# Performance work log

Hardware: AMD Instinct MI355X
Metric: run time of the kernel (lower is better)

The kernel has to match this reference:

```python
import jax, jax.numpy as jnp
import numpy as np

N = 65536   # batch_size * timeseries
D = 512     # feature dim of h_real
K = 64      # n_clusters


def setup_inputs() -> dict:
    key = jax.random.key(0)
    k1, k2 = jax.random.split(key)
    h_real = jax.random.normal(k1, (N, D), dtype=jnp.float32)
    # F is an (approximately) orthogonal projection parameter [N, K].
    F = jax.random.normal(k2, (N, K), dtype=jnp.float32)
    return {"h_real": h_real, "F": F}


def reference(h_real, F):
    # Original: WTW = h h^T (N x N); loss = trace(WTW) - trace(F^T WTW F).
    # Algebraically identical reduced form, never materializing the N x N Gram:
    #   trace(h h^T) = sum(h * h)
    #   trace(F^T h h^T F) = ||F^T h||_F^2
    tr_wtw = jnp.sum(h_real * h_real)
    G = F.T @ h_real                      # [K, D] skinny GEMM
    tr_proj = jnp.sum(G * G)
    return tr_wtw - tr_proj
```

## Files before the change

### kernel.cpp

```cpp
#include <hip/hip_runtime.h>
#include <hip/hip_fp16.h>

#define N_TOT 65536
#define D_DIM 512
#define K_DIM 64
#define NC    32
#define HT_S  40
#define GSZ   (K_DIM * D_DIM)

typedef __bf16   bf16x8 __attribute__((ext_vector_type(8)));
typedef float    f32x4  __attribute__((ext_vector_type(4)));
typedef _Float16 half8  __attribute__((ext_vector_type(8)));

__device__ __forceinline__ unsigned int pack_bf16(float a, float b) {
    union { float f; unsigned int u; } x, y;
    x.f = a; y.f = b;
    unsigned int lo = (x.u + 0x7fffu + ((x.u >> 16) & 1u)) >> 16;
    unsigned int hi = (y.u + 0x7fffu + ((y.u >> 16) & 1u)) >> 16;
    return lo | (hi << 16);
}

extern "C" __global__ void __launch_bounds__(1024)
k1_partial(const float* __restrict__ h, const float* __restrict__ F,
           float* __restrict__ trw_out, unsigned short* __restrict__ gpart,
           float* __restrict__ out, int rowsPerBlock) {
    __shared__ unsigned short ht[2][D_DIM * HT_S];
    __shared__ unsigned short Ft[2][K_DIM * HT_S];
    __shared__ float red[16];

    const int tid = threadIdx.x;
    const int b   = blockIdx.x;
    if (b == 0 && tid == 0) out[0] = 0.0f;

    const int row0    = b * rowsPerBlock;
    const int nChunks = rowsPerBlock / NC;

    const int sd = tid & 511;
    const int sg = tid >> 9;
    const int fk = tid & 63;
    const int fg = (tid >> 6) & 3;
    const int wave = tid >> 6;
    const int lane = tid & 63;
    const int m    = lane & 15;
    const int q    = lane >> 4;

    f32x4 acc[4][2];
    #pragma unroll
    for (int kt = 0; kt < 4; ++kt)
        #pragma unroll
        for (int dt = 0; dt < 2; ++dt)
            acc[kt][dt] = (f32x4){0.f, 0.f, 0.f, 0.f};

    float trw = 0.f;

    auto stage = [&](int c, int p) {
        const int r0 = row0 + c * NC;
        const float* hb = h + (size_t)r0 * D_DIM + sd;
        #pragma unroll
        for (int gi = 0; gi < 2; ++gi) {
            const int g8 = gi * 2 + sg;
            float v[8];
            #pragma unroll
            for (int j = 0; j < 8; ++j) {
                v[j] = hb[(size_t)(g8 * 8 + j) * D_DIM];
                trw += v[j] * v[j];
            }
            uint4 pk;
            pk.x = pack_bf16(v[0], v[1]);
            pk.y = pack_bf16(v[2], v[3]);
            pk.z = pack_bf16(v[4], v[5]);
            pk.w = pack_bf16(v[6], v[7]);
            *(uint4*)&ht[p][sd * HT_S + g8 * 8] = pk;
        }
        if (tid < 256) {
            const float* fb = F + (size_t)r0 * K_DIM + fk;
            float w[8];
            #pragma unroll
            for (int j = 0; j < 8; ++j)
                w[j] = fb[(size_t)(fg * 8 + j) * K_DIM];
            uint4 pk;
            pk.x = pack_bf16(w[0], w[1]);
            pk.y = pack_bf16(w[2], w[3]);
            pk.z = pack_bf16(w[4], w[5]);
            pk.w = pack_bf16(w[6], w[7]);
            *(uint4*)&Ft[p][fk * HT_S + fg * 8] = pk;
        }
    };

    stage(0, 0);

    for (int c = 0; c < nChunks; ++c) {
        __syncthreads();
        if (c + 1 < nChunks) stage(c + 1, (c + 1) & 1);

        const int p = c & 1;
        bf16x8 bfrag[2], afrag[4];
        #pragma unroll
        for (int dt = 0; dt < 2; ++dt)
            bfrag[dt] = *(const bf16x8*)&ht[p][(wave * 32 + dt * 16 + m) * HT_S + q * 8];
        #pragma unroll
        for (int kt = 0; kt < 4; ++kt)
            afrag[kt] = *(const bf16x8*)&Ft[p][(kt * 16 + m) * HT_S + q * 8];
        #pragma unroll
        for (int kt = 0; kt < 4; ++kt)
            #pragma unroll
            for (int dt = 0; dt < 2; ++dt)
                acc[kt][dt] = __builtin_amdgcn_mfma_f32_16x16x32_bf16(
                    afrag[kt], bfrag[dt], acc[kt][dt], 0, 0, 0);
    }

    unsigned short* gp = gpart + (size_t)b * GSZ;
    #pragma unroll
    for (int kt = 0; kt < 4; ++kt)
        #pragma unroll
        for (int dt = 0; dt < 2; ++dt)
            #pragma unroll
            for (int r = 0; r < 4; ++r) {
                const int k = kt * 16 + q * 4 + r;
                const int d = wave * 32 + dt * 16 + m;
                __half hv = __float2half(acc[kt][dt][r]);
                gp[k * D_DIM + d] = *(unsigned short*)&hv;
            }

    #pragma unroll
    for (int off = 32; off > 0; off >>= 1) trw += __shfl_down(trw, off, 64);
    if (lane == 0) red[wave] = trw;
    __syncthreads();
    if (tid == 0) {
        float s = 0.f;
        #pragma unroll
        for (int w = 0; w < 16; ++w) s += red[w];
        trw_out[b] = s;
    }
}

extern "C" __global__ void __launch_bounds__(512)
k2_reduce(const float* __restrict__ trw, const unsigned short* __restrict__ gpart,
          float* __restrict__ out, int P) {
    __shared__ float sh[32 * 16 * 8];
    __shared__ float red2[8];

    const int tid = threadIdx.x;
    const int sub = tid >> 4;
    const int oct = tid & 15;
    const int tt  = blockIdx.x * 16 + oct;

    float g[8];
    #pragma unroll
    for (int j = 0; j < 8; ++j) g[j] = 0.f;

    const unsigned short* base = gpart + (size_t)tt * 8;
    for (int b = sub; b < P; b += 32) {
        half8 v = *(const half8*)(base + (size_t)b * GSZ);
        #pragma unroll
        for (int j = 0; j < 8; ++j) g[j] += (float)v[j];
    }
    #pragma unroll
    for (int j = 0; j < 8; ++j) sh[(sub * 16 + oct) * 8 + j] = g[j];
    __syncthreads();

    float val = 0.f;
    if (tid < 128) {
        const int o2 = tid >> 3, j = tid & 7;
        float s = 0.f;
        #pragma unroll
        for (int sb = 0; sb < 32; ++sb) s += sh[(sb * 16 + o2) * 8 + j];
        val = -s * s;
    } else if (blockIdx.x == 0 && tid - 128 < P) {
        val = trw[tid - 128];
    }

    #pragma unroll
    for (int off = 32; off > 0; off >>= 1) val += __shfl_down(val, off, 64);
    if ((tid & 63) == 0) red2[tid >> 6] = val;
    __syncthreads();
    if (tid == 0) {
        float s = 0.f;
        #pragma unroll
        for (int w = 0; w < 8; ++w) s += red2[w];
        atomicAdd(out, s);
    }
}

extern "C" void kernel_launch(void* const* d_in, const int* in_sizes, int n_in,
                              void* d_out, int out_size, void* d_ws, size_t ws_size,
                              hipStream_t stream) {
    const float* h = (const float*)d_in[0];
    const float* F = (const float*)d_in[1];
    float* out = (float*)d_out;

    int P = 256;
    while (P > 1 && (size_t)4096 + (size_t)P * (GSZ * 2) > ws_size) P >>= 1;
    const int rowsPerBlock = N_TOT / P;

    float* trw = (float*)d_ws;
    unsigned short* gpart = (unsigned short*)((char*)d_ws + 4096);

    hipLaunchKernelGGL(k1_partial, dim3(P), dim3(1024), 0, stream,
                       h, F, trw, gpart, out, rowsPerBlock);
    hipLaunchKernelGGL(k2_reduce, dim3(256), dim3(512), 0, stream,
                       trw, gpart, out, P);
}
```

Baseline: 210.1 us.

## Vectorize global loads in staging and coalesce partial-G writes via LDS

The staging of h and F now uses 128-bit and 64-bit vector loads over four consecutive rows per thread instead of scalar strided loads, and the transposed bf16 tiles are written with 64-bit LDS stores. The per-block fp16 partial G is first gathered in shared memory, reusing the h tile buffer, and then copied to global memory with 16-byte coalesced stores instead of scattered 2-byte writes. The aim is to cut the number of memory instructions and improve coalescing on the bandwidth-bound h read. The cost is an extra barrier and different LDS write patterns that may cause bank conflicts.

```diff
diff --git a/kernel.cpp b/kernel.cpp
--- a/kernel.cpp
+++ b/kernel.cpp
@@ -10,6 +10,7 @@
 
 typedef __bf16   bf16x8 __attribute__((ext_vector_type(8)));
 typedef float    f32x4  __attribute__((ext_vector_type(4)));
+typedef float    f32x2  __attribute__((ext_vector_type(2)));
 typedef _Float16 half8  __attribute__((ext_vector_type(8)));
 
 __device__ __forceinline__ unsigned int pack_bf16(float a, float b) {
@@ -35,10 +36,10 @@
     const int row0    = b * rowsPerBlock;
     const int nChunks = rowsPerBlock / NC;
 
-    const int sd = tid & 511;
-    const int sg = tid >> 9;
-    const int fk = tid & 63;
-    const int fg = (tid >> 6) & 3;
+    const int sd = tid & 127;
+    const int sg = tid >> 7;
+    const int fk = (tid & 31) * 2;
+    const int fg = tid >> 5;
     const int wave = tid >> 6;
     const int lane = tid & 63;
     const int m    = lane & 15;
@@ -55,35 +56,36 @@
 
     auto stage = [&](int c, int p) {
         const int r0 = row0 + c * NC;
-        const float* hb = h + (size_t)r0 * D_DIM + sd;
-        #pragma unroll
-        for (int gi = 0; gi < 2; ++gi) {
-            const int g8 = gi * 2 + sg;
-            float v[8];
-            #pragma unroll
-            for (int j = 0; j < 8; ++j) {
-                v[j] = hb[(size_t)(g8 * 8 + j) * D_DIM];
-                trw += v[j] * v[j];
-            }
-            uint4 pk;
-            pk.x = pack_bf16(v[0], v[1]);
-            pk.y = pack_bf16(v[2], v[3]);
-            pk.z = pack_bf16(v[4], v[5]);
-            pk.w = pack_bf16(v[6], v[7]);
-            *(uint4*)&ht[p][sd * HT_S + g8 * 8] = pk;
+        const float* hb = h + (size_t)(r0 + sg * 4) * D_DIM + sd * 4;
+        f32x4 v[4];
+        #pragma unroll
+        for (int j = 0; j < 4; ++j)
+            v[j] = *(const f32x4*)(hb + (size_t)j * D_DIM);
+        #pragma unroll
+        for (int j = 0; j < 4; ++j)
+            #pragma unroll
+            for (int e = 0; e < 4; ++e)
+                trw += v[j][e] * v[j][e];
+        #pragma unroll
+        for (int e = 0; e < 4; ++e) {
+            uint2 pk;
+            pk.x = pack_bf16(v[0][e], v[1][e]);
+            pk.y = pack_bf16(v[2][e], v[3][e]);
+            *(uint2*)&ht[p][(sd * 4 + e) * HT_S + sg * 4] = pk;
         }
         if (tid < 256) {
-            const float* fb = F + (size_t)r0 * K_DIM + fk;
-            float w[8];
-            #pragma unroll
-            for (int j = 0; j < 8; ++j)
-                w[j] = fb[(size_t)(fg * 8 + j) * K_DIM];
-            uint4 pk;
-            pk.x = pack_bf16(w[0], w[1]);
-            pk.y = pack_bf16(w[2], w[3]);
-            pk.z = pack_bf16(w[4], w[5]);
-            pk.w = pack_bf16(w[6], w[7]);
-            *(uint4*)&Ft[p][fk * HT_S + fg * 8] = pk;
+            const float* fb = F + (size_t)(r0 + fg * 4) * K_DIM + fk;
+            f32x2 w[4];
+            #pragma unroll
+            for (int j = 0; j < 4; ++j)
+                w[j] = *(const f32x2*)(fb + (size_t)j * K_DIM);
+            #pragma unroll
+            for (int e = 0; e < 2; ++e) {
+                uint2 pk;
+                pk.x = pack_bf16(w[0][e], w[1][e]);
+                pk.y = pack_bf16(w[2][e], w[3][e]);
+                *(uint2*)&Ft[p][(fk + e) * HT_S + fg * 4] = pk;
+            }
         }
     };
 
@@ -109,7 +111,8 @@
                     afrag[kt], bfrag[dt], acc[kt][dt], 0, 0, 0);
     }
 
-    unsigned short* gp = gpart + (size_t)b * GSZ;
+    __syncthreads();
+    unsigned short* gt = &ht[0][0];
     #pragma unroll
     for (int kt = 0; kt < 4; ++kt)
         #pragma unroll
@@ -119,13 +122,19 @@
                 const int k = kt * 16 + q * 4 + r;
                 const int d = wave * 32 + dt * 16 + m;
                 __half hv = __float2half(acc[kt][dt][r]);
-                gp[k * D_DIM + d] = *(unsigned short*)&hv;
+                gt[k * D_DIM + d] = *(unsigned short*)&hv;
             }
 
     #pragma unroll
     for (int off = 32; off > 0; off >>= 1) trw += __shfl_down(trw, off, 64);
     if (lane == 0) red[wave] = trw;
     __syncthreads();
+
+    unsigned short* gp = gpart + (size_t)b * GSZ;
+    #pragma unroll
+    for (int it = 0; it < 4; ++it)
+        *(uint4*)(gp + it * 8192 + tid * 8) = *(const uint4*)(gt + it * 8192 + tid * 8);
+
     if (tid == 0) {
         float s = 0.f;
         #pragma unroll
```

New measurement: 212.3 us. Within noise of the previous version (+1.1%).
